# Performance work log

Hardware: AMD Instinct MI355X
Metric: run time of the kernel (lower is better)

The kernel has to match this reference:

```python
import jax, jax.numpy as jnp
import numpy as np

N_NODES = 100000
N_EDGES = 600000
IN_FEATS = 128
HIDDEN = 128


def sage_conv(x, src, dst, w_l, b_l, w_r, num_nodes):
    """PyG SAGEConv with mean aggregation.
    out = mean_{j in N(i)} x_j @ w_l.T + b_l + x_i @ w_r.T
    src/dst: int arrays [E]; messages flow src -> dst.
    """
    msgs = x[src]                                             # [E, F] gather
    summed = jax.ops.segment_sum(msgs, dst, num_segments=num_nodes)  # [N, F]
    ones = jnp.ones((src.shape[0],), dtype=x.dtype)
    deg = jax.ops.segment_sum(ones, dst, num_segments=num_nodes)     # [N]
    agg = summed / jnp.maximum(deg, 1.0)[:, None]             # mean, safe for deg=0
    return agg @ w_l.T + b_l + x @ w_r.T


def setup_inputs() -> dict:
    key = jax.random.key(0)
    ks = jax.random.split(key, 10)

    def glorot(k, shape):
        fan_in = shape[-1]
        bound = 1.0 / np.sqrt(fan_in)
        return jax.random.uniform(k, shape, jnp.float32, -bound, bound)

    x = jax.random.normal(ks[0], (N_NODES, IN_FEATS), dtype=jnp.float32)
    xedge = jax.random.randint(ks[1], (2, N_EDGES), 0, N_NODES, dtype=jnp.int64)
    return {
        "x": x,
        "xedge": xedge,
        # SAGEConv 1 (in_feats -> hidden): lin_l (with bias) + lin_r (no bias)
        "w1_l": glorot(ks[2], (HIDDEN, IN_FEATS)),
        "b1_l": glorot(ks[3], (HIDDEN,)),
        "w1_r": glorot(ks[4], (HIDDEN, IN_FEATS)),
        # SAGEConv 2 (hidden -> hidden)
        "w2_l": glorot(ks[5], (HIDDEN, HIDDEN)),
        "b2_l": glorot(ks[6], (HIDDEN,)),
        "w2_r": glorot(ks[7], (HIDDEN, HIDDEN)),
        # Decoder: Linear(hidden -> hidden)
        "w_dec": glorot(ks[8], (HIDDEN, HIDDEN)),
        "b_dec": glorot(ks[9], (HIDDEN,)),
    }


def reference(x, xedge, w1_l, b1_l, w1_r, w2_l, b2_l, w2_r, w_dec, b_dec):
    src, dst = xedge[0], xedge[1]
    n = x.shape[0]
    h = sage_conv(x, src, dst, w1_l, b1_l, w1_r, n)   # conv1
    h = jax.nn.relu(h)
    # dropout omitted (deterministic eval semantics)
    h = sage_conv(h, src, dst, w2_l, b2_l, w2_r, n)   # conv2 -> encoder output
    dx = h @ w_dec.T + b_dec                          # decoder
    return (h, dx)
```

## Files before the change

kernel.cpp:

```cpp
#include <hip/hip_runtime.h>

typedef __attribute__((ext_vector_type(8))) short bf16x8;
typedef __attribute__((ext_vector_type(4))) float f32x4;
typedef unsigned int uint;
typedef unsigned short ushort;

#define NFEAT 128

__device__ __forceinline__ ushort f2b(float f) {
    uint u = __float_as_uint(f);
    u = (u + 0x7fffu + ((u >> 16) & 1u)) >> 16;
    return (ushort)u;
}

__global__ __launch_bounds__(256) void cvt_bf(const float* __restrict__ in,
                                              ushort* __restrict__ out, long n) {
    long i = ((long)blockIdx.x * 256 + threadIdx.x) * 4;
    if (i >= n) return;
    float4 v = *(const float4*)(in + i);
    ushort4 o;
    o.x = f2b(v.x); o.y = f2b(v.y); o.z = f2b(v.z); o.w = f2b(v.w);
    *(ushort4*)(out + i) = o;
}

__global__ __launch_bounds__(256) void wprep(const float* __restrict__ w1l, const float* __restrict__ w1r,
                                             const float* __restrict__ w2l, const float* __restrict__ w2r,
                                             const float* __restrict__ wd,
                                             ushort* __restrict__ wc1, ushort* __restrict__ wc2,
                                             ushort* __restrict__ wdec) {
    const int b = blockIdx.x;
    if (b < 256) {
        const int i = (b & 127) * 256 + threadIdx.x;
        const int row = i >> 8, col = i & 255;
        const float* wl = (b < 128) ? w1l : w2l;
        const float* wr = (b < 128) ? w1r : w2r;
        ushort* dst = (b < 128) ? wc1 : wc2;
        float v = (col < 128) ? wl[row * 128 + col] : wr[row * 128 + col - 128];
        dst[i] = f2b(v);
    } else {
        const int i = (b - 256) * 256 + threadIdx.x;
        wdec[i] = f2b(wd[i]);
    }
}

__global__ void hist_kernel(const int* __restrict__ dst, int* __restrict__ deg, int E) {
    int e = blockIdx.x * blockDim.x + threadIdx.x;
    if (e < E) atomicAdd(&deg[dst[e]], 1);
}

__global__ __launch_bounds__(256) void scan_blocks(const int* __restrict__ in, int* __restrict__ out,
                                                   int* __restrict__ bsum, int n) {
    __shared__ int lds[256];
    const int t = threadIdx.x;
    const int base = blockIdx.x * 1024 + t * 4;
    int a[4];
#pragma unroll
    for (int q = 0; q < 4; ++q) a[q] = (base + q < n) ? in[base + q] : 0;
    const int tsum = a[0] + a[1] + a[2] + a[3];
    lds[t] = tsum;
    __syncthreads();
    for (int off = 1; off < 256; off <<= 1) {
        int v = (t >= off) ? lds[t - off] : 0;
        __syncthreads();
        lds[t] += v;
        __syncthreads();
    }
    const int excl = lds[t] - tsum;
    if (t == 255) bsum[blockIdx.x] = lds[255];
    int r = excl;
#pragma unroll
    for (int q = 0; q < 4; ++q) {
        if (base + q < n) out[base + q] = r;
        r += a[q];
    }
}

__global__ __launch_bounds__(256) void scan_carry(int* __restrict__ bsum, int nb) {
    __shared__ int lds[256];
    const int t = threadIdx.x;
    const int v = (t < nb) ? bsum[t] : 0;
    lds[t] = v;
    __syncthreads();
    for (int off = 1; off < 256; off <<= 1) {
        int u = (t >= off) ? lds[t - off] : 0;
        __syncthreads();
        lds[t] += u;
        __syncthreads();
    }
    if (t < nb) bsum[t] = lds[t] - v;
}

__global__ void scan_add(int* __restrict__ row_off, int* __restrict__ pos,
                         const int* __restrict__ bsum, int n, int E) {
    const int i = blockIdx.x * blockDim.x + threadIdx.x;
    if (i < n) {
        const int v = row_off[i] + bsum[i >> 10];
        row_off[i] = v;
        pos[i] = v;
    }
    if (i == 0) row_off[n] = E;
}

__global__ void fill_csr(const int* __restrict__ src, const int* __restrict__ dst,
                         int* __restrict__ pos, int* __restrict__ perm, int E) {
    const int e = blockIdx.x * blockDim.x + threadIdx.x;
    if (e < E) {
        const int p = atomicAdd(&pos[dst[e]], 1);
        perm[p] = src[e];
    }
}

__global__ __launch_bounds__(256) void gather_mean_bf(const int* __restrict__ row_off,
                                                      const int* __restrict__ perm,
                                                      const ushort* __restrict__ feat,
                                                      ushort* __restrict__ out, int n) {
    const int node = (blockIdx.x * 256 + threadIdx.x) >> 6;
    if (node >= n) return;
    const int lane = threadIdx.x & 63;
    const int chunk = lane & 15;
    const int sub = lane >> 4;
    const int lo = row_off[node], hi = row_off[node + 1];
    float acc[8] = {0.f, 0.f, 0.f, 0.f, 0.f, 0.f, 0.f, 0.f};
    int i = lo + sub;
    for (; i + 4 < hi; i += 8) {
        const int s0 = perm[i], s1 = perm[i + 4];
        const uint4 v0 = *(const uint4*)(feat + (size_t)s0 * NFEAT + chunk * 8);
        const uint4 v1 = *(const uint4*)(feat + (size_t)s1 * NFEAT + chunk * 8);
        const uint p0[4] = {v0.x, v0.y, v0.z, v0.w};
        const uint p1[4] = {v1.x, v1.y, v1.z, v1.w};
#pragma unroll
        for (int q = 0; q < 4; ++q) {
            acc[2 * q]     += __uint_as_float(p0[q] << 16);
            acc[2 * q + 1] += __uint_as_float(p0[q] & 0xffff0000u);
            acc[2 * q]     += __uint_as_float(p1[q] << 16);
            acc[2 * q + 1] += __uint_as_float(p1[q] & 0xffff0000u);
        }
    }
    if (i < hi) {
        const int s = perm[i];
        const uint4 v = *(const uint4*)(feat + (size_t)s * NFEAT + chunk * 8);
        const uint p[4] = {v.x, v.y, v.z, v.w};
#pragma unroll
        for (int q = 0; q < 4; ++q) {
            acc[2 * q]     += __uint_as_float(p[q] << 16);
            acc[2 * q + 1] += __uint_as_float(p[q] & 0xffff0000u);
        }
    }
#pragma unroll
    for (int q = 0; q < 8; ++q) {
        acc[q] += __shfl_xor(acc[q], 16);
        acc[q] += __shfl_xor(acc[q], 32);
    }
    if (sub == 0) {
        const float inv = 1.0f / fmaxf((float)(hi - lo), 1.0f);
        ushort o[8];
#pragma unroll
        for (int q = 0; q < 8; ++q) o[q] = f2b(acc[q] * inv);
        *(uint4*)(out + (size_t)node * NFEAT + chunk * 8) = *(const uint4*)o;
    }
}

template <bool RELU, bool DEC>
__global__ __launch_bounds__(256) void sage_mfma(
    const ushort* __restrict__ Amean, const ushort* __restrict__ Axin,
    const ushort* __restrict__ Wcat, const float* __restrict__ bias,
    const ushort* __restrict__ Wdec, const float* __restrict__ bdec,
    float* __restrict__ outf, ushort* __restrict__ outb,
    float* __restrict__ dxp, int n)
{
    __shared__ uint4 smem4[2048];
    char* As = (char*)smem4;
    char* Ws = As + 16384;
    const int t = threadIdx.x;
    const int m0 = blockIdx.x * 128;
    const int lane = t & 63;
    const int wid = t >> 6;
    const int lrow = lane & 15;
    const int lq = lane >> 4;

    f32x4 acc[2][8];
#pragma unroll
    for (int m = 0; m < 2; ++m)
#pragma unroll
        for (int nn = 0; nn < 8; ++nn) acc[m][nn] = (f32x4){0.f, 0.f, 0.f, 0.f};

    for (int kt = 0; kt < 4; ++kt) {
        const ushort* Abase = (kt < 2) ? Amean : Axin;
        const int co = (kt & 1) * 64;
#pragma unroll
        for (int i = 0; i < 4; ++i) {
            const int c = t + i * 256;
            const int row = c >> 3, cL = c & 7;
            const int gm = m0 + row;
            uint4 v = make_uint4(0, 0, 0, 0);
            if (gm < n) v = *(const uint4*)((const char*)Abase + ((size_t)gm * NFEAT + co) * 2 + cL * 16);
            *(uint4*)(As + row * 128 + ((cL * 16) ^ ((row & 7) << 4))) = v;
        }
#pragma unroll
        for (int i = 0; i < 4; ++i) {
            const int c = t + i * 256;
            const int row = c >> 3, cL = c & 7;
            const uint4 v = *(const uint4*)((const char*)Wcat + ((size_t)row * 256 + kt * 64) * 2 + cL * 16);
            *(uint4*)(Ws + row * 128 + ((cL * 16) ^ ((row & 7) << 4))) = v;
        }
        __syncthreads();
#pragma unroll
        for (int ks = 0; ks < 2; ++ks) {
            bf16x8 af[2], bfr[8];
#pragma unroll
            for (int m = 0; m < 2; ++m) {
                const int row = wid * 32 + m * 16 + lrow;
                af[m] = *(const bf16x8*)(As + row * 128 + (((ks * 4 + lq) * 16) ^ ((row & 7) << 4)));
            }
#pragma unroll
            for (int nn = 0; nn < 8; ++nn) {
                const int row = nn * 16 + lrow;
                bfr[nn] = *(const bf16x8*)(Ws + row * 128 + (((ks * 4 + lq) * 16) ^ ((row & 7) << 4)));
            }
#pragma unroll
            for (int m = 0; m < 2; ++m)
#pragma unroll
                for (int nn = 0; nn < 8; ++nn)
                    acc[m][nn] = __builtin_amdgcn_mfma_f32_16x16x32_bf16(bfr[nn], af[m], acc[m][nn], 0, 0, 0);
        }
        __syncthreads();
    }
    char* Lh = As;
#pragma unroll
    for (int m = 0; m < 2; ++m) {
        const int row = wid * 32 + m * 16 + lrow;
        const int grow = m0 + row;
#pragma unroll
        for (int nn = 0; nn < 8; ++nn) {
            const int colb = nn * 16 + lq * 4;
            const float4 bv = *(const float4*)(bias + colb);
            float v0 = acc[m][nn][0] + bv.x;
            float v1 = acc[m][nn][1] + bv.y;
            float v2 = acc[m][nn][2] + bv.z;
            float v3 = acc[m][nn][3] + bv.w;
            if (RELU) {
                v0 = fmaxf(v0, 0.f); v1 = fmaxf(v1, 0.f);
                v2 = fmaxf(v2, 0.f); v3 = fmaxf(v3, 0.f);
            }
            ushort4 ob;
            ob.x = f2b(v0); ob.y = f2b(v1); ob.z = f2b(v2); ob.w = f2b(v3);
            if (grow < n) {
                if (outf) *(float4*)(outf + (size_t)grow * NFEAT + colb) = make_float4(v0, v1, v2, v3);
                if (outb) *(ushort4*)(outb + (size_t)grow * NFEAT + colb) = ob;
            }
            if (DEC)
                *(ushort4*)(Lh + row * 256 + ((colb * 2) ^ ((row & 7) << 4))) = ob;
        }
    }
    if (DEC) {
        f32x4 acc2[2][8];
#pragma unroll
        for (int m = 0; m < 2; ++m)
#pragma unroll
            for (int nn = 0; nn < 8; ++nn) acc2[m][nn] = (f32x4){0.f, 0.f, 0.f, 0.f};
#pragma unroll
        for (int ks = 0; ks < 4; ++ks) {
            bf16x8 af2[2], bf2[8];
#pragma unroll
            for (int m = 0; m < 2; ++m) {
                const int row = wid * 32 + m * 16 + lrow;
                af2[m] = *(const bf16x8*)(Lh + row * 256 + ((ks * 64 + lq * 16) ^ ((row & 7) << 4)));
            }
#pragma unroll
            for (int nn = 0; nn < 8; ++nn)
                bf2[nn] = *(const bf16x8*)(Wdec + (size_t)(nn * 16 + lrow) * NFEAT + ks * 32 + lq * 8);
#pragma unroll
            for (int m = 0; m < 2; ++m)
#pragma unroll
                for (int nn = 0; nn < 8; ++nn)
                    acc2[m][nn] = __builtin_amdgcn_mfma_f32_16x16x32_bf16(bf2[nn], af2[m], acc2[m][nn], 0, 0, 0);
        }
#pragma unroll
        for (int m = 0; m < 2; ++m) {
            const int grow = m0 + wid * 32 + m * 16 + lrow;
            if (grow < n) {
#pragma unroll
                for (int nn = 0; nn < 8; ++nn) {
                    const int colb = nn * 16 + lq * 4;
                    const float4 bv = *(const float4*)(bdec + colb);
                    *(float4*)(dxp + (size_t)grow * NFEAT + colb) =
                        make_float4(acc2[m][nn][0] + bv.x, acc2[m][nn][1] + bv.y,
                                    acc2[m][nn][2] + bv.z, acc2[m][nn][3] + bv.w);
                }
            }
        }
    }
}

extern "C" void kernel_launch(void* const* d_in, const int* in_sizes, int n_in,
                              void* d_out, int out_size, void* d_ws, size_t ws_size,
                              hipStream_t stream) {
    const float* x     = (const float*)d_in[0];
    const int*   xedge = (const int*)d_in[1];
    const float* w1_l  = (const float*)d_in[2];
    const float* b1_l  = (const float*)d_in[3];
    const float* w1_r  = (const float*)d_in[4];
    const float* w2_l  = (const float*)d_in[5];
    const float* b2_l  = (const float*)d_in[6];
    const float* w2_r  = (const float*)d_in[7];
    const float* w_dec = (const float*)d_in[8];
    const float* b_dec = (const float*)d_in[9];

    const int N = in_sizes[0] / NFEAT;
    const int E = in_sizes[1] / 2;
    const int* src = xedge;
    const int* dst = xedge + E;

    float* h_out = (float*)d_out;
    float* dxp   = h_out + (size_t)N * NFEAT;

    char* ws = (char*)d_ws;
    ushort* x_bf    = (ushort*)ws;
    ushort* h1_bf   = x_bf   + (size_t)N * NFEAT;
    ushort* mean_bf = h1_bf  + (size_t)N * NFEAT;
    ushort* wc1     = mean_bf + (size_t)N * NFEAT;
    ushort* wc2     = wc1 + 128 * 256;
    ushort* wdec    = wc2 + 128 * 256;
    int* deg        = (int*)(wdec + 128 * 128);
    int* row_off    = deg + N;
    int* pos        = row_off + (N + 1);
    int* bsum       = pos + N;
    int* perm       = bsum + 256;

    const long nx = (long)N * NFEAT;
    cvt_bf<<<(int)((nx / 4 + 255) / 256), 256, 0, stream>>>(x, x_bf, nx);
    wprep<<<320, 256, 0, stream>>>(w1_l, w1_r, w2_l, w2_r, w_dec, wc1, wc2, wdec);

    hipMemsetAsync(deg, 0, (size_t)N * sizeof(int), stream);
    hist_kernel<<<(E + 255) / 256, 256, 0, stream>>>(dst, deg, E);
    const int nb = (N + 1023) / 1024;
    scan_blocks<<<nb, 256, 0, stream>>>(deg, row_off, bsum, N);
    scan_carry<<<1, 256, 0, stream>>>(bsum, nb);
    scan_add<<<(N + 255) / 256, 256, 0, stream>>>(row_off, pos, bsum, N, E);
    fill_csr<<<(E + 255) / 256, 256, 0, stream>>>(src, dst, pos, perm, E);

    const int gb = (N + 127) / 128;

    gather_mean_bf<<<(N + 3) / 4, 256, 0, stream>>>(row_off, perm, x_bf, mean_bf, N);
    sage_mfma<true, false><<<gb, 256, 0, stream>>>(mean_bf, x_bf, wc1, b1_l,
                                                   nullptr, nullptr, nullptr, h1_bf, nullptr, N);

    gather_mean_bf<<<(N + 3) / 4, 256, 0, stream>>>(row_off, perm, h1_bf, mean_bf, N);
    sage_mfma<false, true><<<gb, 256, 0, stream>>>(mean_bf, h1_bf, wc2, b2_l,
                                                   wdec, b_dec, h_out, nullptr, dxp, N);

    (void)n_in; (void)out_size; (void)ws_size;
}
```

Baseline: 226.2 us.

## Fuse neighbor mean gather into SAGE MFMA kernel, keep mean tile in LDS

Each SAGE layer now gathers the neighbor mean for its 128-row tile directly into LDS and feeds it to the MFMA, dropping the separate gather kernel and the global mean buffer round trip. Weight and self-feature fragments are loaded straight from global memory instead of being staged through shared memory, which removes the per-k-tile syncthreads. The cost is fewer blocks doing the gather (a wave serially walks 32 nodes) and less latency hiding. The uncached global reads of weights per wave also add traffic.

```diff
diff --git a/kernel.cpp b/kernel.cpp
--- a/kernel.cpp
+++ b/kernel.cpp
@@ -110,67 +110,17 @@
     }
 }
 
-__global__ __launch_bounds__(256) void gather_mean_bf(const int* __restrict__ row_off,
-                                                      const int* __restrict__ perm,
-                                                      const ushort* __restrict__ feat,
-                                                      ushort* __restrict__ out, int n) {
-    const int node = (blockIdx.x * 256 + threadIdx.x) >> 6;
-    if (node >= n) return;
-    const int lane = threadIdx.x & 63;
-    const int chunk = lane & 15;
-    const int sub = lane >> 4;
-    const int lo = row_off[node], hi = row_off[node + 1];
-    float acc[8] = {0.f, 0.f, 0.f, 0.f, 0.f, 0.f, 0.f, 0.f};
-    int i = lo + sub;
-    for (; i + 4 < hi; i += 8) {
-        const int s0 = perm[i], s1 = perm[i + 4];
-        const uint4 v0 = *(const uint4*)(feat + (size_t)s0 * NFEAT + chunk * 8);
-        const uint4 v1 = *(const uint4*)(feat + (size_t)s1 * NFEAT + chunk * 8);
-        const uint p0[4] = {v0.x, v0.y, v0.z, v0.w};
-        const uint p1[4] = {v1.x, v1.y, v1.z, v1.w};
-#pragma unroll
-        for (int q = 0; q < 4; ++q) {
-            acc[2 * q]     += __uint_as_float(p0[q] << 16);
-            acc[2 * q + 1] += __uint_as_float(p0[q] & 0xffff0000u);
-            acc[2 * q]     += __uint_as_float(p1[q] << 16);
-            acc[2 * q + 1] += __uint_as_float(p1[q] & 0xffff0000u);
-        }
-    }
-    if (i < hi) {
-        const int s = perm[i];
-        const uint4 v = *(const uint4*)(feat + (size_t)s * NFEAT + chunk * 8);
-        const uint p[4] = {v.x, v.y, v.z, v.w};
-#pragma unroll
-        for (int q = 0; q < 4; ++q) {
-            acc[2 * q]     += __uint_as_float(p[q] << 16);
-            acc[2 * q + 1] += __uint_as_float(p[q] & 0xffff0000u);
-        }
-    }
-#pragma unroll
-    for (int q = 0; q < 8; ++q) {
-        acc[q] += __shfl_xor(acc[q], 16);
-        acc[q] += __shfl_xor(acc[q], 32);
-    }
-    if (sub == 0) {
-        const float inv = 1.0f / fmaxf((float)(hi - lo), 1.0f);
-        ushort o[8];
-#pragma unroll
-        for (int q = 0; q < 8; ++q) o[q] = f2b(acc[q] * inv);
-        *(uint4*)(out + (size_t)node * NFEAT + chunk * 8) = *(const uint4*)o;
-    }
-}
-
 template <bool RELU, bool DEC>
-__global__ __launch_bounds__(256) void sage_mfma(
-    const ushort* __restrict__ Amean, const ushort* __restrict__ Axin,
-    const ushort* __restrict__ Wcat, const float* __restrict__ bias,
+__global__ __launch_bounds__(256) void sage_fused(
+    const int* __restrict__ row_off, const int* __restrict__ perm,
+    const ushort* __restrict__ feat, const ushort* __restrict__ Wcat,
+    const float* __restrict__ bias,
     const ushort* __restrict__ Wdec, const float* __restrict__ bdec,
     float* __restrict__ outf, ushort* __restrict__ outb,
     float* __restrict__ dxp, int n)
 {
-    __shared__ uint4 smem4[2048];
-    char* As = (char*)smem4;
-    char* Ws = As + 16384;
+    __shared__ uint4 LmeanBuf[2048];
+    char* Lmean = (char*)LmeanBuf;
     const int t = threadIdx.x;
     const int m0 = blockIdx.x * 128;
     const int lane = t & 63;
@@ -178,54 +128,90 @@
     const int lrow = lane & 15;
     const int lq = lane >> 4;
 
+    {
+        const int chunk = lane & 15;
+        const int sub = lane >> 4;
+        for (int r = 0; r < 32; ++r) {
+            const int row = wid * 32 + r;
+            const int node = m0 + row;
+            if (node >= n) break;
+            const int lo = row_off[node], hi = row_off[node + 1];
+            float acc[8] = {0.f, 0.f, 0.f, 0.f, 0.f, 0.f, 0.f, 0.f};
+            int i = lo + sub;
+            for (; i + 4 < hi; i += 8) {
+                const int s0 = perm[i], s1 = perm[i + 4];
+                const uint4 v0 = *(const uint4*)(feat + (size_t)s0 * NFEAT + chunk * 8);
+                const uint4 v1 = *(const uint4*)(feat + (size_t)s1 * NFEAT + chunk * 8);
+                const uint p0[4] = {v0.x, v0.y, v0.z, v0.w};
+                const uint p1[4] = {v1.x, v1.y, v1.z, v1.w};
+#pragma unroll
+                for (int q = 0; q < 4; ++q) {
+                    acc[2 * q]     += __uint_as_float(p0[q] << 16);
+                    acc[2 * q + 1] += __uint_as_float(p0[q] & 0xffff0000u);
+                    acc[2 * q]     += __uint_as_float(p1[q] << 16);
+                    acc[2 * q + 1] += __uint_as_float(p1[q] & 0xffff0000u);
+                }
+            }
+            if (i < hi) {
+                const int s = perm[i];
+                const uint4 v = *(const uint4*)(feat + (size_t)s * NFEAT + chunk * 8);
+                const uint p[4] = {v.x, v.y, v.z, v.w};
+#pragma unroll
+                for (int q = 0; q < 4; ++q) {
+                    acc[2 * q]     += __uint_as_float(p[q] << 16);
+                    acc[2 * q + 1] += __uint_as_float(p[q] & 0xffff0000u);
+                }
+            }
+#pragma unroll
+            for (int q = 0; q < 8; ++q) {
+                acc[q] += __shfl_xor(acc[q], 16);
+                acc[q] += __shfl_xor(acc[q], 32);
+            }
+            if (sub == 0) {
+                const float inv = 1.0f / fmaxf((float)(hi - lo), 1.0f);
+                ushort o[8] __attribute__((aligned(16)));
+#pragma unroll
+                for (int q = 0; q < 8; ++q) o[q] = f2b(acc[q] * inv);
+                *(uint4*)(Lmean + row * 256 + ((chunk * 16) ^ ((row & 7) << 4))) = *(const uint4*)o;
+            }
+        }
+    }
+
     f32x4 acc[2][8];
 #pragma unroll
     for (int m = 0; m < 2; ++m)
 #pragma unroll
         for (int nn = 0; nn < 8; ++nn) acc[m][nn] = (f32x4){0.f, 0.f, 0.f, 0.f};
 
+#pragma unroll
     for (int kt = 0; kt < 4; ++kt) {
-        const ushort* Abase = (kt < 2) ? Amean : Axin;
-        const int co = (kt & 1) * 64;
-#pragma unroll
-        for (int i = 0; i < 4; ++i) {
-            const int c = t + i * 256;
-            const int row = c >> 3, cL = c & 7;
-            const int gm = m0 + row;
-            uint4 v = make_uint4(0, 0, 0, 0);
-            if (gm < n) v = *(const uint4*)((const char*)Abase + ((size_t)gm * NFEAT + co) * 2 + cL * 16);
-            *(uint4*)(As + row * 128 + ((cL * 16) ^ ((row & 7) << 4))) = v;
-        }
-#pragma unroll
-        for (int i = 0; i < 4; ++i) {
-            const int c = t + i * 256;
-            const int row = c >> 3, cL = c & 7;
-            const uint4 v = *(const uint4*)((const char*)Wcat + ((size_t)row * 256 + kt * 64) * 2 + cL * 16);
-            *(uint4*)(Ws + row * 128 + ((cL * 16) ^ ((row & 7) << 4))) = v;
-        }
-        __syncthreads();
 #pragma unroll
         for (int ks = 0; ks < 2; ++ks) {
             bf16x8 af[2], bfr[8];
 #pragma unroll
             for (int m = 0; m < 2; ++m) {
                 const int row = wid * 32 + m * 16 + lrow;
-                af[m] = *(const bf16x8*)(As + row * 128 + (((ks * 4 + lq) * 16) ^ ((row & 7) << 4)));
-            }
-#pragma unroll
-            for (int nn = 0; nn < 8; ++nn) {
-                const int row = nn * 16 + lrow;
-                bfr[nn] = *(const bf16x8*)(Ws + row * 128 + (((ks * 4 + lq) * 16) ^ ((row & 7) << 4)));
-            }
+                if (kt < 2) {
+                    af[m] = *(const bf16x8*)(Lmean + row * 256 +
+                                             ((kt * 128 + ks * 64 + lq * 16) ^ ((row & 7) << 4)));
+                } else {
+                    int grow = m0 + row;
+                    if (grow >= n) grow = n - 1;
+                    af[m] = *(const bf16x8*)(feat + (size_t)grow * NFEAT + (kt & 1) * 64 + ks * 32 + lq * 8);
+                }
+            }
+#pragma unroll
+            for (int nn = 0; nn < 8; ++nn)
+                bfr[nn] = *(const bf16x8*)(Wcat + (size_t)(nn * 16 + lrow) * 256 + kt * 64 + ks * 32 + lq * 8);
 #pragma unroll
             for (int m = 0; m < 2; ++m)
 #pragma unroll
                 for (int nn = 0; nn < 8; ++nn)
                     acc[m][nn] = __builtin_amdgcn_mfma_f32_16x16x32_bf16(bfr[nn], af[m], acc[m][nn], 0, 0, 0);
         }
-        __syncthreads();
-    }
-    char* Lh = As;
+    }
+
+    char* Lh = Lmean;
 #pragma unroll
     for (int m = 0; m < 2; ++m) {
         const int row = wid * 32 + m * 16 + lrow;
@@ -316,9 +302,8 @@
 
     char* ws = (char*)d_ws;
     ushort* x_bf    = (ushort*)ws;
-    ushort* h1_bf   = x_bf   + (size_t)N * NFEAT;
-    ushort* mean_bf = h1_bf  + (size_t)N * NFEAT;
-    ushort* wc1     = mean_bf + (size_t)N * NFEAT;
+    ushort* h1_bf   = x_bf  + (size_t)N * NFEAT;
+    ushort* wc1     = h1_bf + (size_t)N * NFEAT;
     ushort* wc2     = wc1 + 128 * 256;
     ushort* wdec    = wc2 + 128 * 256;
     int* deg        = (int*)(wdec + 128 * 128);
@@ -341,13 +326,11 @@
 
     const int gb = (N + 127) / 128;
 
-    gather_mean_bf<<<(N + 3) / 4, 256, 0, stream>>>(row_off, perm, x_bf, mean_bf, N);
-    sage_mfma<true, false><<<gb, 256, 0, stream>>>(mean_bf, x_bf, wc1, b1_l,
-                                                   nullptr, nullptr, nullptr, h1_bf, nullptr, N);
-
-    gather_mean_bf<<<(N + 3) / 4, 256, 0, stream>>>(row_off, perm, h1_bf, mean_bf, N);
-    sage_mfma<false, true><<<gb, 256, 0, stream>>>(mean_bf, h1_bf, wc2, b2_l,
-                                                   wdec, b_dec, h_out, nullptr, dxp, N);
+    sage_fused<true, false><<<gb, 256, 0, stream>>>(row_off, perm, x_bf, wc1, b1_l,
+                                                    nullptr, nullptr, nullptr, h1_bf, nullptr, N);
+
+    sage_fused<false, true><<<gb, 256, 0, stream>>>(row_off, perm, h1_bf, wc2, b2_l,
+                                                    wdec, b_dec, h_out, nullptr, dxp, N);
 
     (void)n_in; (void)out_size; (void)ws_size;
 }
```

Result: slower. 363.3 us (+60.6%).

## Fuse prep kernels with histogram and use 16 lanes per node in gather

Applied to the files above, without the earlier changes.

Merges the x bf16 conversion, weight packing and degree histogram into one multi-role kernel, cutting two launches. The mean-gather kernel now gives each node 16 lanes instead of 64, so each lane loops over all neighbours with 4 loads in flight and no cross-lane shuffle reduction is needed. This quadruples the nodes per block and drops idle lanes for low-degree nodes (about 6 edges on average), at the cost of longer serial loops for high-degree nodes.

```diff
diff --git a/kernel.cpp b/kernel.cpp
--- a/kernel.cpp
+++ b/kernel.cpp
@@ -13,39 +13,39 @@
     return (ushort)u;
 }
 
-__global__ __launch_bounds__(256) void cvt_bf(const float* __restrict__ in,
-                                              ushort* __restrict__ out, long n) {
-    long i = ((long)blockIdx.x * 256 + threadIdx.x) * 4;
-    if (i >= n) return;
-    float4 v = *(const float4*)(in + i);
-    ushort4 o;
-    o.x = f2b(v.x); o.y = f2b(v.y); o.z = f2b(v.z); o.w = f2b(v.w);
-    *(ushort4*)(out + i) = o;
-}
-
-__global__ __launch_bounds__(256) void wprep(const float* __restrict__ w1l, const float* __restrict__ w1r,
-                                             const float* __restrict__ w2l, const float* __restrict__ w2r,
-                                             const float* __restrict__ wd,
-                                             ushort* __restrict__ wc1, ushort* __restrict__ wc2,
-                                             ushort* __restrict__ wdec) {
+__global__ __launch_bounds__(256) void prep(
+    const float* __restrict__ x, ushort* __restrict__ x_bf, long nx,
+    const float* __restrict__ w1l, const float* __restrict__ w1r,
+    const float* __restrict__ w2l, const float* __restrict__ w2r,
+    const float* __restrict__ wd,
+    ushort* __restrict__ wc1, ushort* __restrict__ wc2, ushort* __restrict__ wdec,
+    const int* __restrict__ dst, int* __restrict__ deg, int E, int nCvt)
+{
     const int b = blockIdx.x;
-    if (b < 256) {
-        const int i = (b & 127) * 256 + threadIdx.x;
+    if (b < nCvt) {
+        long i = ((long)b * 256 + threadIdx.x) * 4;
+        if (i < nx) {
+            float4 v = *(const float4*)(x + i);
+            ushort4 o;
+            o.x = f2b(v.x); o.y = f2b(v.y); o.z = f2b(v.z); o.w = f2b(v.w);
+            *(ushort4*)(x_bf + i) = o;
+        }
+    } else if (b < nCvt + 256) {
+        const int bb = b - nCvt;
+        const int i = (bb & 127) * 256 + threadIdx.x;
         const int row = i >> 8, col = i & 255;
-        const float* wl = (b < 128) ? w1l : w2l;
-        const float* wr = (b < 128) ? w1r : w2r;
-        ushort* dst = (b < 128) ? wc1 : wc2;
+        const float* wl = (bb < 128) ? w1l : w2l;
+        const float* wr = (bb < 128) ? w1r : w2r;
+        ushort* dstw = (bb < 128) ? wc1 : wc2;
         float v = (col < 128) ? wl[row * 128 + col] : wr[row * 128 + col - 128];
-        dst[i] = f2b(v);
+        dstw[i] = f2b(v);
+    } else if (b < nCvt + 320) {
+        const int i = (b - nCvt - 256) * 256 + threadIdx.x;
+        wdec[i] = f2b(wd[i]);
     } else {
-        const int i = (b - 256) * 256 + threadIdx.x;
-        wdec[i] = f2b(wd[i]);
-    }
-}
-
-__global__ void hist_kernel(const int* __restrict__ dst, int* __restrict__ deg, int E) {
-    int e = blockIdx.x * blockDim.x + threadIdx.x;
-    if (e < E) atomicAdd(&deg[dst[e]], 1);
+        const int e = (b - nCvt - 320) * 256 + threadIdx.x;
+        if (e < E) atomicAdd(&deg[dst[e]], 1);
+    }
 }
 
 __global__ __launch_bounds__(256) void scan_blocks(const int* __restrict__ in, int* __restrict__ out,
@@ -114,29 +114,31 @@
                                                       const int* __restrict__ perm,
                                                       const ushort* __restrict__ feat,
                                                       ushort* __restrict__ out, int n) {
-    const int node = (blockIdx.x * 256 + threadIdx.x) >> 6;
+    const int node = (blockIdx.x * 256 + threadIdx.x) >> 4;
     if (node >= n) return;
-    const int lane = threadIdx.x & 63;
-    const int chunk = lane & 15;
-    const int sub = lane >> 4;
+    const int chunk = threadIdx.x & 15;
     const int lo = row_off[node], hi = row_off[node + 1];
     float acc[8] = {0.f, 0.f, 0.f, 0.f, 0.f, 0.f, 0.f, 0.f};
-    int i = lo + sub;
-    for (; i + 4 < hi; i += 8) {
-        const int s0 = perm[i], s1 = perm[i + 4];
+    int i = lo;
+    for (; i + 3 < hi; i += 4) {
+        const int s0 = perm[i], s1 = perm[i + 1], s2 = perm[i + 2], s3 = perm[i + 3];
         const uint4 v0 = *(const uint4*)(feat + (size_t)s0 * NFEAT + chunk * 8);
         const uint4 v1 = *(const uint4*)(feat + (size_t)s1 * NFEAT + chunk * 8);
+        const uint4 v2 = *(const uint4*)(feat + (size_t)s2 * NFEAT + chunk * 8);
+        const uint4 v3 = *(const uint4*)(feat + (size_t)s3 * NFEAT + chunk * 8);
         const uint p0[4] = {v0.x, v0.y, v0.z, v0.w};
         const uint p1[4] = {v1.x, v1.y, v1.z, v1.w};
+        const uint p2[4] = {v2.x, v2.y, v2.z, v2.w};
+        const uint p3[4] = {v3.x, v3.y, v3.z, v3.w};
 #pragma unroll
         for (int q = 0; q < 4; ++q) {
-            acc[2 * q]     += __uint_as_float(p0[q] << 16);
-            acc[2 * q + 1] += __uint_as_float(p0[q] & 0xffff0000u);
-            acc[2 * q]     += __uint_as_float(p1[q] << 16);
-            acc[2 * q + 1] += __uint_as_float(p1[q] & 0xffff0000u);
-        }
-    }
-    if (i < hi) {
+            acc[2 * q]     += __uint_as_float(p0[q] << 16) + __uint_as_float(p1[q] << 16)
+                            + __uint_as_float(p2[q] << 16) + __uint_as_float(p3[q] << 16);
+            acc[2 * q + 1] += __uint_as_float(p0[q] & 0xffff0000u) + __uint_as_float(p1[q] & 0xffff0000u)
+                            + __uint_as_float(p2[q] & 0xffff0000u) + __uint_as_float(p3[q] & 0xffff0000u);
+        }
+    }
+    for (; i < hi; ++i) {
         const int s = perm[i];
         const uint4 v = *(const uint4*)(feat + (size_t)s * NFEAT + chunk * 8);
         const uint p[4] = {v.x, v.y, v.z, v.w};
@@ -146,18 +148,11 @@
             acc[2 * q + 1] += __uint_as_float(p[q] & 0xffff0000u);
         }
     }
-#pragma unroll
-    for (int q = 0; q < 8; ++q) {
-        acc[q] += __shfl_xor(acc[q], 16);
-        acc[q] += __shfl_xor(acc[q], 32);
-    }
-    if (sub == 0) {
-        const float inv = 1.0f / fmaxf((float)(hi - lo), 1.0f);
-        ushort o[8];
-#pragma unroll
-        for (int q = 0; q < 8; ++q) o[q] = f2b(acc[q] * inv);
-        *(uint4*)(out + (size_t)node * NFEAT + chunk * 8) = *(const uint4*)o;
-    }
+    const float inv = 1.0f / fmaxf((float)(hi - lo), 1.0f);
+    ushort o[8] __attribute__((aligned(16)));
+#pragma unroll
+    for (int q = 0; q < 8; ++q) o[q] = f2b(acc[q] * inv);
+    *(uint4*)(out + (size_t)node * NFEAT + chunk * 8) = *(const uint4*)o;
 }
 
 template <bool RELU, bool DEC>
@@ -327,25 +322,27 @@
     int* bsum       = pos + N;
     int* perm       = bsum + 256;
 
+    hipMemsetAsync(deg, 0, (size_t)N * sizeof(int), stream);
     const long nx = (long)N * NFEAT;
-    cvt_bf<<<(int)((nx / 4 + 255) / 256), 256, 0, stream>>>(x, x_bf, nx);
-    wprep<<<320, 256, 0, stream>>>(w1_l, w1_r, w2_l, w2_r, w_dec, wc1, wc2, wdec);
-
-    hipMemsetAsync(deg, 0, (size_t)N * sizeof(int), stream);
-    hist_kernel<<<(E + 255) / 256, 256, 0, stream>>>(dst, deg, E);
+    const int nCvt = (int)((nx / 4 + 255) / 256);
+    const int histB = (E + 255) / 256;
+    prep<<<nCvt + 320 + histB, 256, 0, stream>>>(x, x_bf, nx, w1_l, w1_r, w2_l, w2_r, w_dec,
+                                                 wc1, wc2, wdec, dst, deg, E, nCvt);
+
     const int nb = (N + 1023) / 1024;
     scan_blocks<<<nb, 256, 0, stream>>>(deg, row_off, bsum, N);
     scan_carry<<<1, 256, 0, stream>>>(bsum, nb);
     scan_add<<<(N + 255) / 256, 256, 0, stream>>>(row_off, pos, bsum, N, E);
-    fill_csr<<<(E + 255) / 256, 256, 0, stream>>>(src, dst, pos, perm, E);
+    fill_csr<<<histB, 256, 0, stream>>>(src, dst, pos, perm, E);
 
     const int gb = (N + 127) / 128;
-
-    gather_mean_bf<<<(N + 3) / 4, 256, 0, stream>>>(row_off, perm, x_bf, mean_bf, N);
+    const int ggb = (N * 16 + 255) / 256;
+
+    gather_mean_bf<<<ggb, 256, 0, stream>>>(row_off, perm, x_bf, mean_bf, N);
     sage_mfma<true, false><<<gb, 256, 0, stream>>>(mean_bf, x_bf, wc1, b1_l,
                                                    nullptr, nullptr, nullptr, h1_bf, nullptr, N);
 
-    gather_mean_bf<<<(N + 3) / 4, 256, 0, stream>>>(row_off, perm, h1_bf, mean_bf, N);
+    gather_mean_bf<<<ggb, 256, 0, stream>>>(row_off, perm, h1_bf, mean_bf, N);
     sage_mfma<false, true><<<gb, 256, 0, stream>>>(mean_bf, h1_bf, wc2, b2_l,
                                                    wdec, b_dec, h_out, nullptr, dxp, N);
 
```

New measurement: 209.3 us. 1.08x faster.
